# Performance work log

Hardware: AMD Instinct MI355X
Metric: run time of the kernel (lower is better)

Reference implementation:

```python
import jax, jax.numpy as jnp
import numpy as np

B, T, D = 8, 1024, 1024
DMAX = 8
MAX_FRAMES = T * DMAX  # static upper bound on expanded length
SPEED = 1.0
EPS = 1e-5


def setup_inputs() -> dict:
    key = jax.random.key(0)
    ks = jax.random.split(key, 8)
    s = 0.02
    return {
        "x": jax.random.normal(ks[0], (B, T, D), dtype=jnp.float32),
        "target_durations": jax.random.randint(ks[1], (B, T), 0, DMAX, dtype=jnp.int32),
        "w1": jax.random.normal(ks[2], (D, D, 3), dtype=jnp.float32) * s,
        "b1": jnp.zeros((D,), jnp.float32),
        "g1": jnp.ones((D,), jnp.float32),
        "be1": jnp.zeros((D,), jnp.float32),
        "w2": jax.random.normal(ks[3], (D, D, 3), dtype=jnp.float32) * s,
        "b2": jnp.zeros((D,), jnp.float32),
        "g2": jnp.ones((D,), jnp.float32),
        "be2": jnp.zeros((D,), jnp.float32),
        "wl": jax.random.normal(ks[4], (1, D), dtype=jnp.float32) * s,
        "bl": jnp.zeros((1,), jnp.float32),
    }


def _conv1d(h, w, b):
    # h: [B, C, T], w: [O, I, K], padding=1 (same)
    o = jax.lax.conv_general_dilated(h, w, window_strides=(1,), padding=((1, 1),),
                                     dimension_numbers=("NCH", "OIH", "NCH"))
    return o + b[None, :, None]


def _ln(h, g, b):
    # layernorm over last dim
    m = jnp.mean(h, axis=-1, keepdims=True)
    v = jnp.mean(jnp.square(h - m), axis=-1, keepdims=True)
    return (h - m) * jax.lax.rsqrt(v + EPS) * g + b


def _predictor(x, w1, b1, g1, be1, w2, b2, g2, be2, wl, bl):
    h = jnp.transpose(x, (0, 2, 1))                  # [B, D, T]
    h = jax.nn.relu(_conv1d(h, w1, b1))
    h = _ln(jnp.transpose(h, (0, 2, 1)), g1, be1)    # [B, T, D]
    h = jnp.transpose(h, (0, 2, 1))
    h = jax.nn.relu(_conv1d(h, w2, b2))
    h = _ln(jnp.transpose(h, (0, 2, 1)), g2, be2)    # [B, T, D]
    return (h @ wl.T + bl)[..., 0]                   # [B, T] log-durations


def _expand(x, durations):
    # vectorized length regulation: token index per output frame via searchsorted
    cum = jnp.cumsum(durations, axis=1)              # [B, T]
    frames = jnp.arange(MAX_FRAMES)                  # [F]
    tok = jax.vmap(lambda c: jnp.searchsorted(c, frames, side="right"))(cum)  # [B, F]
    valid = frames[None, :] < cum[:, -1:]            # [B, F]
    tok = jnp.minimum(tok, x.shape[1] - 1)
    out = jnp.take_along_axis(x, tok[:, :, None], axis=1)  # [B, F, D]
    return jnp.where(valid[:, :, None], out, 0.0)


def reference(x, target_durations, w1, b1, g1, be1, w2, b2, g2, be2, wl, bl):
    log_d = _predictor(x, w1, b1, g1, be1, w2, b2, g2, be2, wl, bl)
    _pred = jnp.maximum(jnp.round(jnp.exp(log_d) / SPEED).astype(jnp.int32), 1)
    durations = target_durations  # target path overrides prediction
    padded = _expand(x, durations)
    return padded, durations
```

## Files before the change

### kernel.cpp

```cpp
#include <hip/hip_runtime.h>


#define B_ 8
#define T_ 1024
#define D_ 1024
#define F_ 8192
#define DV4 (D_ / 4)
#define ZROWS 32
#define NSCAT (B_ * T_)
#define NZERO ((B_ * F_) / ZROWS)

typedef float vfloat4 __attribute__((ext_vector_type(4)));

__global__ void __launch_bounds__(1024) dur_scan_kernel(
    const int* __restrict__ dur,
    int* __restrict__ cum,
    float* __restrict__ out_dur)
{
    __shared__ int s[T_];
    const int b = blockIdx.x;
    const int t = threadIdx.x;

    const int d = dur[b * T_ + t];
    out_dur[b * T_ + t] = (float)d;

    s[t] = d;
    __syncthreads();
    #pragma unroll
    for (int off = 1; off < T_; off <<= 1) {
        int v = (t >= off) ? s[t - off] : 0;
        __syncthreads();
        s[t] += v;
        __syncthreads();
    }
    cum[b * T_ + t] = s[t];
}

__global__ void __launch_bounds__(256) expand_fused_kernel(
    const float* __restrict__ x,
    const int* __restrict__ cum,
    float* __restrict__ out)
{
    const int idx = blockIdx.x;
    if (idx < NSCAT) {
        const int bt = idx;
        const int b  = bt >> 10;
        const int t  = bt & (T_ - 1);

        const int c1 = cum[bt];
        const int c0 = t ? cum[bt - 1] : 0;
        if (c0 == c1) return;

        const vfloat4 v =
            reinterpret_cast<const vfloat4*>(x)[(size_t)bt * DV4 + threadIdx.x];
        vfloat4* dstb = reinterpret_cast<vfloat4*>(out)
                      + (size_t)b * F_ * DV4 + threadIdx.x;
        for (int r = c0; r < c1; ++r)
            dstb[(size_t)r * DV4] = v;
    } else {
        const int chunk = (idx - NSCAT) * ZROWS;
        const int b     = chunk >> 13;
        const int f0    = chunk & (F_ - 1);
        const int total = cum[b * T_ + T_ - 1];
        if (f0 + ZROWS <= total) return;

        vfloat4* dstb = reinterpret_cast<vfloat4*>(out)
                      + (size_t)chunk * DV4 + threadIdx.x;
        #pragma unroll 4
        for (int r = 0; r < ZROWS; ++r) {
            if (f0 + r >= total)
                dstb[(size_t)r * DV4] = (vfloat4)(0.f);
        }
    }
}

extern "C" void kernel_launch(void* const* d_in, const int* in_sizes, int n_in,
                              void* d_out, int out_size, void* d_ws, size_t ws_size,
                              hipStream_t stream)
{
    const float* x   = (const float*)d_in[0];
    const int*   dur = (const int*)d_in[1];

    float* out     = (float*)d_out;
    float* out_dur = out + (size_t)B_ * F_ * D_;
    int*   cum     = (int*)d_ws;

    dur_scan_kernel<<<B_, T_, 0, stream>>>(dur, cum, out_dur);
    expand_fused_kernel<<<NSCAT + NZERO, 256, 0, stream>>>(x, cum, out);
}
```

Before: 324.3 us.

## Replace scatter expansion with per-frame gather using precomputed token map

The scan kernel now writes a frame-to-token map (with -1 for padding frames) instead of cumulative sums. The expansion kernel switches from a per-token scatter plus a separate zero-fill pass to a uniform per-frame gather, one wave per output row, using nontemporal stores. This balances work across blocks and removes the serial per-token write loop and the partial zero-fill chunks. In exchange, source rows get re-read once per duplicated frame, and the scan kernel does extra serial writes per token.

```diff
diff --git a/kernel.cpp b/kernel.cpp
--- a/kernel.cpp
+++ b/kernel.cpp
@@ -6,15 +6,14 @@
 #define D_ 1024
 #define F_ 8192
 #define DV4 (D_ / 4)
-#define ZROWS 32
-#define NSCAT (B_ * T_)
-#define NZERO ((B_ * F_) / ZROWS)
+#define WPB 16
+#define NBLK ((B_ * F_) / WPB)
 
 typedef float vfloat4 __attribute__((ext_vector_type(4)));
 
-__global__ void __launch_bounds__(1024) dur_scan_kernel(
+__global__ void __launch_bounds__(1024) dur_scan_tok_kernel(
     const int* __restrict__ dur,
-    int* __restrict__ cum,
+    int* __restrict__ tok,
     float* __restrict__ out_dur)
 {
     __shared__ int s[T_];
@@ -33,44 +32,49 @@
         s[t] += v;
         __syncthreads();
     }
-    cum[b * T_ + t] = s[t];
+    const int c1    = s[t];
+    const int c0    = t ? s[t - 1] : 0;
+    const int total = s[T_ - 1];
+
+    int* tokb = tok + b * F_;
+    for (int f = c0; f < c1; ++f)
+        tokb[f] = t;
+    for (int f = total + t; f < F_; f += T_)
+        tokb[f] = -1;
 }
 
-__global__ void __launch_bounds__(256) expand_fused_kernel(
+__global__ void __launch_bounds__(1024) expand_gather_kernel(
     const float* __restrict__ x,
-    const int* __restrict__ cum,
+    const int* __restrict__ tok,
     float* __restrict__ out)
 {
-    const int idx = blockIdx.x;
-    if (idx < NSCAT) {
-        const int bt = idx;
-        const int b  = bt >> 10;
-        const int t  = bt & (T_ - 1);
+    const int wave = threadIdx.x >> 6;
+    const int lane = threadIdx.x & 63;
+    const int row  = blockIdx.x * WPB + wave;
+    const int b    = row >> 13;
 
-        const int c1 = cum[bt];
-        const int c0 = t ? cum[bt - 1] : 0;
-        if (c0 == c1) return;
+    const int tk = tok[row];
 
-        const vfloat4 v =
-            reinterpret_cast<const vfloat4*>(x)[(size_t)bt * DV4 + threadIdx.x];
-        vfloat4* dstb = reinterpret_cast<vfloat4*>(out)
-                      + (size_t)b * F_ * DV4 + threadIdx.x;
-        for (int r = c0; r < c1; ++r)
-            dstb[(size_t)r * DV4] = v;
+    vfloat4* dst = reinterpret_cast<vfloat4*>(out)
+                 + (size_t)row * DV4 + lane;
+
+    if (tk >= 0) {
+        const vfloat4* src = reinterpret_cast<const vfloat4*>(x)
+                           + (size_t)(b * T_ + tk) * DV4 + lane;
+        const vfloat4 v0 = src[0];
+        const vfloat4 v1 = src[64];
+        const vfloat4 v2 = src[128];
+        const vfloat4 v3 = src[192];
+        __builtin_nontemporal_store(v0, dst);
+        __builtin_nontemporal_store(v1, dst + 64);
+        __builtin_nontemporal_store(v2, dst + 128);
+        __builtin_nontemporal_store(v3, dst + 192);
     } else {
-        const int chunk = (idx - NSCAT) * ZROWS;
-        const int b     = chunk >> 13;
-        const int f0    = chunk & (F_ - 1);
-        const int total = cum[b * T_ + T_ - 1];
-        if (f0 + ZROWS <= total) return;
-
-        vfloat4* dstb = reinterpret_cast<vfloat4*>(out)
-                      + (size_t)chunk * DV4 + threadIdx.x;
-        #pragma unroll 4
-        for (int r = 0; r < ZROWS; ++r) {
-            if (f0 + r >= total)
-                dstb[(size_t)r * DV4] = (vfloat4)(0.f);
-        }
+        const vfloat4 z = {0.f, 0.f, 0.f, 0.f};
+        __builtin_nontemporal_store(z, dst);
+        __builtin_nontemporal_store(z, dst + 64);
+        __builtin_nontemporal_store(z, dst + 128);
+        __builtin_nontemporal_store(z, dst + 192);
     }
 }
 
@@ -83,8 +87,8 @@
 
     float* out     = (float*)d_out;
     float* out_dur = out + (size_t)B_ * F_ * D_;
-    int*   cum     = (int*)d_ws;
+    int*   tok     = (int*)d_ws;
 
-    dur_scan_kernel<<<B_, T_, 0, stream>>>(dur, cum, out_dur);
-    expand_fused_kernel<<<NSCAT + NZERO, 256, 0, stream>>>(x, cum, out);
+    dur_scan_tok_kernel<<<B_, T_, 0, stream>>>(dur, tok, out_dur);
+    expand_gather_kernel<<<NBLK, 1024, 0, stream>>>(x, tok, out);
 }
```

Result: no change. 327.7 us (+1.0%).
